# Kernel tuning notes

Hardware: AMD Instinct MI355X
Metric: run time of the kernel (lower is better)

The kernel has to match this reference:

```python
import jax, jax.numpy as jnp
import numpy as np

N = 4096      # num nodes
F = 64        # input feature dim
H = 8         # head_num
D = 8         # att_embedding_size


def setup_inputs() -> dict:
    key = jax.random.key(0)
    k1, k2, k3, k4, k5, k6 = jax.random.split(key, 6)
    X = jax.random.normal(k1, (N, F), dtype=jnp.float32)
    # sparse-ish binary adjacency with self loops (avg degree ~ 41)
    A = (jax.random.uniform(k2, (N, N)) < 0.01).astype(jnp.float32)
    A = jnp.maximum(A, jnp.eye(N, dtype=jnp.float32))
    # glorot-uniform-ish parameter init
    lim_w = np.sqrt(6.0 / (F + H * D)).astype(np.float32)
    W = jax.random.uniform(k3, (F, H * D), minval=-lim_w, maxval=lim_w, dtype=jnp.float32)
    lim_a = np.sqrt(6.0 / (1 + H * D)).astype(np.float32)
    att_self = jax.random.uniform(k4, (H, D), minval=-lim_a, maxval=lim_a, dtype=jnp.float32)
    att_neigh = jax.random.uniform(k5, (H, D), minval=-lim_a, maxval=lim_a, dtype=jnp.float32)
    bias = jnp.zeros((H, D), dtype=jnp.float32)
    return {"X": X, "A": A, "W": W, "att_self": att_self, "att_neigh": att_neigh, "bias": bias}


def reference(X, A, W, att_self, att_neigh, bias):
    # features: [N, H, D]
    feats = (X @ W).reshape(-1, H, D)
    # additive attention logits per node/head: [N, H]
    a_self = jnp.einsum('nhd,hd->nh', feats, att_self)
    a_neigh = jnp.einsum('nhd,hd->nh', feats, att_neigh)
    # scores[h, i, j] = a_self[i, h] + a_neigh[j, h]  -> [H, N, N]
    scores = a_self.T[:, :, None] + a_neigh.T[:, None, :]
    scores = jax.nn.leaky_relu(scores, negative_slope=0.2)
    # adjacency mask: -1e10 where no edge
    scores = scores + (-1e10 * (1.0 - A))[None, :, :]
    attn = jax.nn.softmax(scores, axis=-1)           # [H, N, N]
    # aggregate: [H, N, N] x [N, H, D] -> [N, H, D]
    out = jnp.einsum('hij,jhd->ihd', attn, feats)
    out = out + bias[None, :, :]                     # use_bias
    out = out.reshape(-1, H * D)                     # reduction='concat'
    return jax.nn.relu(out)                          # activation=relu
```

## Files before the change

### kernel.cpp

```cpp
#include <hip/hip_runtime.h>
#include <hip/hip_bf16.h>

#define NNODES 4096
#define NF 64
#define NH 8
#define ND 8
#define HD 64

__device__ __forceinline__ float ldv(const void* p, int i, bool f32) {
    return f32 ? ((const float*)p)[i]
               : __bfloat162float(((const __hip_bfloat16*)p)[i]);
}

__device__ __forceinline__ bool a_is_f32(const void* A) {
    return *(const unsigned int*)A == 0x3F800000u;
}

__global__ __launch_bounds__(256) void gat_feats(
    const void* __restrict__ X,
    const void* __restrict__ W,
    const void* __restrict__ att_self,
    const void* __restrict__ att_neigh,
    const void* __restrict__ A,
    float* __restrict__ feats,
    float* __restrict__ a_self,
    float* __restrict__ a_neigh)
{
    const bool f32 = a_is_f32(A);
    __shared__ float Wl[NF][HD];
    __shared__ float Xl[4][NF];

    const int t = threadIdx.x;

    #pragma unroll
    for (int k = 0; k < 16; ++k) {
        int idx = t + k * 256;
        Wl[idx >> 6][idx & 63] = ldv(W, idx, f32);
    }

    const int n0 = blockIdx.x * 4;
    const int r = t >> 6;
    const int c = t & 63;
    Xl[r][c] = ldv(X, (n0 + r) * NF + c, f32);
    __syncthreads();

    float acc = 0.f;
    #pragma unroll
    for (int k = 0; k < NF; ++k)
        acc = fmaf(Xl[r][k], Wl[k][c], acc);

    const int n = n0 + r;
    feats[n * HD + c] = acc;

    const int d = c & 7;
    const int h = c >> 3;
    float vs = acc * ldv(att_self, c, f32);
    float vn = acc * ldv(att_neigh, c, f32);
    #pragma unroll
    for (int off = 1; off < 8; off <<= 1) {
        vs += __shfl_xor(vs, off, 64);
        vn += __shfl_xor(vn, off, 64);
    }
    if (d == 0) {
        a_self[n * NH + h]  = vs;
        a_neigh[n * NH + h] = vn;
    }
}

__global__ __launch_bounds__(256) void gat_aggr(
    const void* __restrict__ A,
    const float* __restrict__ feats,
    const float* __restrict__ a_self_g,
    const float* __restrict__ a_neigh,
    const void* __restrict__ bias,
    float* __restrict__ out)
{
    const int i = blockIdx.x;
    const int t = threadIdx.x;
    const bool f32 = a_is_f32(A);
    const int wave = t >> 6, lane = t & 63;

    __shared__ unsigned short elist[NNODES];
    __shared__ int wtot[4];
    __shared__ float red[4][HD];
    __shared__ float dsh[4][NH];

    unsigned int bits = 0;
    if (f32) {
        const uint4* ap = (const uint4*)((const float*)A + (size_t)i * NNODES + t * 16);
        #pragma unroll
        for (int q = 0; q < 4; ++q) {
            uint4 p = ap[q];
            if (p.x) bits |= 1u << (4 * q + 0);
            if (p.y) bits |= 1u << (4 * q + 1);
            if (p.z) bits |= 1u << (4 * q + 2);
            if (p.w) bits |= 1u << (4 * q + 3);
        }
    } else {
        const uint4* ap = (const uint4*)((const unsigned short*)A + (size_t)i * NNODES + t * 16);
        uint4 p0 = ap[0], p1 = ap[1];
        unsigned int w0[4] = {p0.x, p0.y, p0.z, p0.w};
        unsigned int w1[4] = {p1.x, p1.y, p1.z, p1.w};
        #pragma unroll
        for (int q = 0; q < 4; ++q) {
            if (w0[q] & 0x0000ffffu) bits |= 1u << (2 * q);
            if (w0[q] & 0xffff0000u) bits |= 1u << (2 * q + 1);
            if (w1[q] & 0x0000ffffu) bits |= 1u << (8 + 2 * q);
            if (w1[q] & 0xffff0000u) bits |= 1u << (8 + 2 * q + 1);
        }
    }

    int cnt = __popc(bits);
    int incl = cnt;
    #pragma unroll
    for (int off = 1; off < 64; off <<= 1) {
        int nn = __shfl_up(incl, off, 64);
        if (lane >= off) incl += nn;
    }
    if (lane == 63) wtot[wave] = incl;
    __syncthreads();
    int base = 0;
    #pragma unroll
    for (int w = 0; w < 4; ++w) if (w < wave) base += wtot[w];
    const int nE = wtot[0] + wtot[1] + wtot[2] + wtot[3];
    int off0 = base + (incl - cnt);
    unsigned int mb = bits;
    while (mb) {
        int b = __ffs(mb) - 1; mb &= mb - 1;
        elist[off0++] = (unsigned short)(t * 16 + b);
    }
    __syncthreads();

    const int c = lane;
    const int h = c >> 3, d = c & 7;
    const float ash = a_self_g[i * NH + h];
    float acc = 0.f, den = 0.f;

    const int chunk = (nE + 3) >> 2;
    int e = wave * chunk;
    const int eEnd = min(nE, e + chunk);

    for (; e + 4 <= eEnd; e += 4) {
        int j0 = elist[e], j1 = elist[e + 1], j2 = elist[e + 2], j3 = elist[e + 3];
        float f0 = feats[j0 * HD + c];
        float f1 = feats[j1 * HD + c];
        float f2 = feats[j2 * HD + c];
        float f3 = feats[j3 * HD + c];
        float a0 = a_neigh[j0 * NH + h];
        float a1 = a_neigh[j1 * NH + h];
        float a2 = a_neigh[j2 * NH + h];
        float a3 = a_neigh[j3 * NH + h];
        float s0 = ash + a0; s0 = (s0 >= 0.f) ? s0 : 0.2f * s0; float w0 = __expf(s0);
        float s1 = ash + a1; s1 = (s1 >= 0.f) ? s1 : 0.2f * s1; float w1 = __expf(s1);
        float s2 = ash + a2; s2 = (s2 >= 0.f) ? s2 : 0.2f * s2; float w2 = __expf(s2);
        float s3 = ash + a3; s3 = (s3 >= 0.f) ? s3 : 0.2f * s3; float w3 = __expf(s3);
        acc = fmaf(w0, f0, acc);
        acc = fmaf(w1, f1, acc);
        acc = fmaf(w2, f2, acc);
        acc = fmaf(w3, f3, acc);
        den += (w0 + w1) + (w2 + w3);
    }
    for (; e < eEnd; ++e) {
        int j = elist[e];
        float s = ash + a_neigh[j * NH + h];
        s = (s >= 0.f) ? s : 0.2f * s;
        float wt = __expf(s);
        acc = fmaf(wt, feats[j * HD + c], acc);
        den += wt;
    }

    red[wave][c] = acc;
    if (d == 0) dsh[wave][h] = den;
    __syncthreads();

    if (t < HD) {
        float tot = red[0][t] + red[1][t] + red[2][t] + red[3][t];
        int hh = t >> 3;
        float dd = dsh[0][hh] + dsh[1][hh] + dsh[2][hh] + dsh[3][hh];
        float v = tot / dd + ldv(bias, t, f32);
        out[(size_t)i * HD + t] = fmaxf(v, 0.f);
    }
}

extern "C" void kernel_launch(void* const* d_in, const int* in_sizes, int n_in,
                              void* d_out, int out_size, void* d_ws, size_t ws_size,
                              hipStream_t stream) {
    const void* X         = d_in[0];
    const void* A         = d_in[1];
    const void* W         = d_in[2];
    const void* att_self  = d_in[3];
    const void* att_neigh = d_in[4];
    const void* bias      = d_in[5];
    float* out = (float*)d_out;

    float* feats   = (float*)d_ws;
    float* a_self  = feats  + NNODES * HD;
    float* a_neigh = a_self + NNODES * NH;

    gat_feats<<<NNODES / 4, 256, 0, stream>>>(X, W, att_self, att_neigh, A,
                                              feats, a_self, a_neigh);
    gat_aggr<<<NNODES, 256, 0, stream>>>(A, feats, a_self, a_neigh, bias, out);
}
```

Baseline: 29.93 us.

## Aggregate raw X per head then project through W, skip feats buffer

The first kernel now computes only the attention logits, by folding att vectors into W (U = W·att) so each node's logits are a 64-length dot with X. The aggregation kernel gathers neighbor X rows instead of precomputed feats, accumulates a per-head weighted sum of X (8 heads × 64 features), then multiplies by W held in shared memory. This removes the N×64 feats write/read, but each block now loads W and does an extra 8×64×64 matmul, with 8x more accumulator registers and more shared memory.

```diff
diff --git a/kernel.cpp b/kernel.cpp
--- a/kernel.cpp
+++ b/kernel.cpp
@@ -12,67 +12,78 @@
                : __bfloat162float(((const __hip_bfloat16*)p)[i]);
 }
 
+__device__ __forceinline__ void ld8(const void* base, int idx, bool f32, float* o) {
+    if (f32) {
+        const float4* p = (const float4*)((const float*)base + idx);
+        float4 a = p[0], b = p[1];
+        o[0]=a.x; o[1]=a.y; o[2]=a.z; o[3]=a.w;
+        o[4]=b.x; o[5]=b.y; o[6]=b.z; o[7]=b.w;
+    } else {
+        uint4 u = *(const uint4*)((const unsigned short*)base + idx);
+        unsigned int ws[4] = {u.x, u.y, u.z, u.w};
+        #pragma unroll
+        for (int q = 0; q < 4; ++q) {
+            o[2*q]   = __uint_as_float(ws[q] << 16);
+            o[2*q+1] = __uint_as_float(ws[q] & 0xffff0000u);
+        }
+    }
+}
+
 __device__ __forceinline__ bool a_is_f32(const void* A) {
     return *(const unsigned int*)A == 0x3F800000u;
 }
 
-__global__ __launch_bounds__(256) void gat_feats(
+__global__ __launch_bounds__(256) void gat_logits(
+    const void* __restrict__ X, const void* __restrict__ W,
+    const void* __restrict__ att_s, const void* __restrict__ att_n,
+    const void* __restrict__ A,
+    float* __restrict__ a_self, float* __restrict__ a_neigh)
+{
+    const bool f32 = a_is_f32(A);
+    __shared__ float UV[NF * 17];
+    __shared__ float Xl[16 * 65];
+    const int t = threadIdx.x;
+
+    #pragma unroll
+    for (int rep = 0; rep < 4; ++rep) {
+        int idx = t + rep * 256;
+        int f = idx >> 4, c6 = idx & 15;
+        int h = c6 & 7;
+        float wv[8];
+        ld8(W, f * HD + h * ND, f32, wv);
+        const void* att = (c6 < 8) ? att_s : att_n;
+        float s = 0.f;
+        #pragma unroll
+        for (int d = 0; d < 8; ++d)
+            s = fmaf(wv[d], ldv(att, h * 8 + d, f32), s);
+        UV[f * 17 + c6] = s;
+    }
+    if (t < 128) {
+        int row = t >> 3, col = (t & 7) * 8;
+        float xv[8];
+        ld8(X, (blockIdx.x * 16 + row) * NF + col, f32, xv);
+        #pragma unroll
+        for (int k = 0; k < 8; ++k) Xl[row * 65 + col + k] = xv[k];
+    }
+    __syncthreads();
+
+    const int r = t >> 4, c6 = t & 15;
+    float s = 0.f;
+    #pragma unroll
+    for (int f = 0; f < NF; ++f)
+        s = fmaf(Xl[r * 65 + f], UV[f * 17 + c6], s);
+    const int n = blockIdx.x * 16 + r;
+    if (c6 < 8) a_self[n * NH + c6]       = s;
+    else        a_neigh[n * NH + (c6-8)]  = s;
+}
+
+__global__ __launch_bounds__(256) void gat_aggr(
+    const void* __restrict__ A,
     const void* __restrict__ X,
     const void* __restrict__ W,
-    const void* __restrict__ att_self,
-    const void* __restrict__ att_neigh,
-    const void* __restrict__ A,
-    float* __restrict__ feats,
-    float* __restrict__ a_self,
-    float* __restrict__ a_neigh)
-{
-    const bool f32 = a_is_f32(A);
-    __shared__ float Wl[NF][HD];
-    __shared__ float Xl[4][NF];
-
-    const int t = threadIdx.x;
-
-    #pragma unroll
-    for (int k = 0; k < 16; ++k) {
-        int idx = t + k * 256;
-        Wl[idx >> 6][idx & 63] = ldv(W, idx, f32);
-    }
-
-    const int n0 = blockIdx.x * 4;
-    const int r = t >> 6;
-    const int c = t & 63;
-    Xl[r][c] = ldv(X, (n0 + r) * NF + c, f32);
-    __syncthreads();
-
-    float acc = 0.f;
-    #pragma unroll
-    for (int k = 0; k < NF; ++k)
-        acc = fmaf(Xl[r][k], Wl[k][c], acc);
-
-    const int n = n0 + r;
-    feats[n * HD + c] = acc;
-
-    const int d = c & 7;
-    const int h = c >> 3;
-    float vs = acc * ldv(att_self, c, f32);
-    float vn = acc * ldv(att_neigh, c, f32);
-    #pragma unroll
-    for (int off = 1; off < 8; off <<= 1) {
-        vs += __shfl_xor(vs, off, 64);
-        vn += __shfl_xor(vn, off, 64);
-    }
-    if (d == 0) {
-        a_self[n * NH + h]  = vs;
-        a_neigh[n * NH + h] = vn;
-    }
-}
-
-__global__ __launch_bounds__(256) void gat_aggr(
-    const void* __restrict__ A,
-    const float* __restrict__ feats,
+    const void* __restrict__ bias,
     const float* __restrict__ a_self_g,
     const float* __restrict__ a_neigh,
-    const void* __restrict__ bias,
     float* __restrict__ out)
 {
     const int i = blockIdx.x;
@@ -80,10 +91,23 @@
     const bool f32 = a_is_f32(A);
     const int wave = t >> 6, lane = t & 63;
 
-    __shared__ unsigned short elist[NNODES];
+    __shared__ float Wlf[NF * HD];
+    __shared__ float shbuf[2048];
+    __shared__ float agg[NH * 65];
+    __shared__ float dsh[4][NH];
+    __shared__ float denT[NH];
+    __shared__ float fin[4][HD];
     __shared__ int wtot[4];
-    __shared__ float red[4][HD];
-    __shared__ float dsh[4][NH];
+    unsigned short* elist = (unsigned short*)shbuf;
+    float* red = shbuf;
+
+    {
+        float wv[16];
+        ld8(W, t * 16,     f32, wv);
+        ld8(W, t * 16 + 8, f32, wv + 8);
+        #pragma unroll
+        for (int k = 0; k < 16; ++k) Wlf[t * 16 + k] = wv[k];
+    }
 
     unsigned int bits = 0;
     if (f32) {
@@ -91,10 +115,10 @@
         #pragma unroll
         for (int q = 0; q < 4; ++q) {
             uint4 p = ap[q];
-            if (p.x) bits |= 1u << (4 * q + 0);
-            if (p.y) bits |= 1u << (4 * q + 1);
-            if (p.z) bits |= 1u << (4 * q + 2);
-            if (p.w) bits |= 1u << (4 * q + 3);
+            if (p.x) bits |= 1u << (4*q+0);
+            if (p.y) bits |= 1u << (4*q+1);
+            if (p.z) bits |= 1u << (4*q+2);
+            if (p.w) bits |= 1u << (4*q+3);
         }
     } else {
         const uint4* ap = (const uint4*)((const unsigned short*)A + (size_t)i * NNODES + t * 16);
@@ -103,10 +127,10 @@
         unsigned int w1[4] = {p1.x, p1.y, p1.z, p1.w};
         #pragma unroll
         for (int q = 0; q < 4; ++q) {
-            if (w0[q] & 0x0000ffffu) bits |= 1u << (2 * q);
-            if (w0[q] & 0xffff0000u) bits |= 1u << (2 * q + 1);
-            if (w1[q] & 0x0000ffffu) bits |= 1u << (8 + 2 * q);
-            if (w1[q] & 0xffff0000u) bits |= 1u << (8 + 2 * q + 1);
+            if (w0[q] & 0x0000ffffu) bits |= 1u << (2*q);
+            if (w0[q] & 0xffff0000u) bits |= 1u << (2*q+1);
+            if (w1[q] & 0x0000ffffu) bits |= 1u << (8+2*q);
+            if (w1[q] & 0xffff0000u) bits |= 1u << (8+2*q+1);
         }
     }
 
@@ -131,53 +155,74 @@
     }
     __syncthreads();
 
-    const int c = lane;
-    const int h = c >> 3, d = c & 7;
+    const int h = lane >> 3, fs = lane & 7;
     const float ash = a_self_g[i * NH + h];
-    float acc = 0.f, den = 0.f;
+    float acc[8] = {0,0,0,0,0,0,0,0};
+    float den = 0.f;
 
     const int chunk = (nE + 3) >> 2;
     int e = wave * chunk;
     const int eEnd = min(nE, e + chunk);
 
-    for (; e + 4 <= eEnd; e += 4) {
-        int j0 = elist[e], j1 = elist[e + 1], j2 = elist[e + 2], j3 = elist[e + 3];
-        float f0 = feats[j0 * HD + c];
-        float f1 = feats[j1 * HD + c];
-        float f2 = feats[j2 * HD + c];
-        float f3 = feats[j3 * HD + c];
-        float a0 = a_neigh[j0 * NH + h];
-        float a1 = a_neigh[j1 * NH + h];
-        float a2 = a_neigh[j2 * NH + h];
-        float a3 = a_neigh[j3 * NH + h];
-        float s0 = ash + a0; s0 = (s0 >= 0.f) ? s0 : 0.2f * s0; float w0 = __expf(s0);
-        float s1 = ash + a1; s1 = (s1 >= 0.f) ? s1 : 0.2f * s1; float w1 = __expf(s1);
-        float s2 = ash + a2; s2 = (s2 >= 0.f) ? s2 : 0.2f * s2; float w2 = __expf(s2);
-        float s3 = ash + a3; s3 = (s3 >= 0.f) ? s3 : 0.2f * s3; float w3 = __expf(s3);
-        acc = fmaf(w0, f0, acc);
-        acc = fmaf(w1, f1, acc);
-        acc = fmaf(w2, f2, acc);
-        acc = fmaf(w3, f3, acc);
-        den += (w0 + w1) + (w2 + w3);
-    }
-    for (; e < eEnd; ++e) {
+    for (; e + 2 <= eEnd; e += 2) {
+        int j0 = elist[e], j1 = elist[e + 1];
+        float x0[8], x1[8];
+        ld8(X, j0 * NF + fs * 8, f32, x0);
+        ld8(X, j1 * NF + fs * 8, f32, x1);
+        float an0 = a_neigh[j0 * NH + h];
+        float an1 = a_neigh[j1 * NH + h];
+        float s0 = ash + an0; s0 = (s0 >= 0.f) ? s0 : 0.2f * s0; float w0 = __expf(s0);
+        float s1 = ash + an1; s1 = (s1 >= 0.f) ? s1 : 0.2f * s1; float w1 = __expf(s1);
+        #pragma unroll
+        for (int k = 0; k < 8; ++k) {
+            acc[k] = fmaf(w0, x0[k], acc[k]);
+            acc[k] = fmaf(w1, x1[k], acc[k]);
+        }
+        den += w0 + w1;
+    }
+    if (e < eEnd) {
         int j = elist[e];
+        float xv[8];
+        ld8(X, j * NF + fs * 8, f32, xv);
         float s = ash + a_neigh[j * NH + h];
         s = (s >= 0.f) ? s : 0.2f * s;
         float wt = __expf(s);
-        acc = fmaf(wt, feats[j * HD + c], acc);
+        #pragma unroll
+        for (int k = 0; k < 8; ++k) acc[k] = fmaf(wt, xv[k], acc[k]);
         den += wt;
     }
-
-    red[wave][c] = acc;
-    if (d == 0) dsh[wave][h] = den;
+    __syncthreads();
+
+    #pragma unroll
+    for (int k = 0; k < 8; ++k) red[wave * 512 + lane * 8 + k] = acc[k];
+    if (fs == 0) dsh[wave][h] = den;
+    __syncthreads();
+
+    #pragma unroll
+    for (int rr = 0; rr < 2; ++rr) {
+        int idx = t * 2 + rr;
+        int hh = idx >> 6, ff = idx & 63;
+        float v = red[idx] + red[512 + idx] + red[1024 + idx] + red[1536 + idx];
+        agg[hh * 65 + ff] = v;
+    }
+    if (t < NH) denT[t] = dsh[0][t] + dsh[1][t] + dsh[2][t] + dsh[3][t];
+    __syncthreads();
+
+    {
+        const int c = lane, hh = c >> 3;
+        float p = 0.f;
+        #pragma unroll
+        for (int f0 = 0; f0 < 16; ++f0) {
+            int f = wave * 16 + f0;
+            p = fmaf(agg[hh * 65 + f], Wlf[f * HD + c], p);
+        }
+        fin[wave][c] = p;
+    }
     __syncthreads();
 
     if (t < HD) {
-        float tot = red[0][t] + red[1][t] + red[2][t] + red[3][t];
-        int hh = t >> 3;
-        float dd = dsh[0][hh] + dsh[1][hh] + dsh[2][hh] + dsh[3][hh];
-        float v = tot / dd + ldv(bias, t, f32);
+        float tot = fin[0][t] + fin[1][t] + fin[2][t] + fin[3][t];
+        float v = tot / denT[t >> 3] + ldv(bias, t, f32);
         out[(size_t)i * HD + t] = fmaxf(v, 0.f);
     }
 }
@@ -193,11 +238,10 @@
     const void* bias      = d_in[5];
     float* out = (float*)d_out;
 
-    float* feats   = (float*)d_ws;
-    float* a_self  = feats  + NNODES * HD;
+    float* a_self  = (float*)d_ws;
     float* a_neigh = a_self + NNODES * NH;
 
-    gat_feats<<<NNODES / 4, 256, 0, stream>>>(X, W, att_self, att_neigh, A,
-                                              feats, a_self, a_neigh);
-    gat_aggr<<<NNODES, 256, 0, stream>>>(A, feats, a_self, a_neigh, bias, out);
-}
+    gat_logits<<<NNODES / 16, 256, 0, stream>>>(X, W, att_self, att_neigh, A,
+                                                a_self, a_neigh);
+    gat_aggr<<<NNODES, 256, 0, stream>>>(A, X, W, bias, a_self, a_neigh, out);
+}
```

Measured after the change: 38.82 us. +29.7%, slower.

## Process one node per wavefront using ballot-driven edge iteration without shared memory

Applied to the files above, without the earlier changes.

The aggregation kernel now assigns one destination row to each 64-lane wavefront instead of one row per 256-thread block. Each lane scans 64 adjacency entries into a 64-bit mask, and the edges are walked with ballot/shuffle bit iteration. This removes the shared-memory edge list, the prefix scan, the block barriers and the cross-wave reduction. The cost is that each wave processes all ~41 edges serially and each lane issues more adjacency loads, with less parallelism per row.

```diff
diff --git a/kernel.cpp b/kernel.cpp
--- a/kernel.cpp
+++ b/kernel.cpp
@@ -6,6 +6,8 @@
 #define NH 8
 #define ND 8
 #define HD 64
+
+typedef unsigned long long u64;
 
 __device__ __forceinline__ float ldv(const void* p, int i, bool f32) {
     return f32 ? ((const float*)p)[i]
@@ -75,111 +77,96 @@
     const void* __restrict__ bias,
     float* __restrict__ out)
 {
-    const int i = blockIdx.x;
-    const int t = threadIdx.x;
     const bool f32 = a_is_f32(A);
-    const int wave = t >> 6, lane = t & 63;
+    const int lane = threadIdx.x & 63;
+    const int i = (blockIdx.x << 2) + (threadIdx.x >> 6);
 
-    __shared__ unsigned short elist[NNODES];
-    __shared__ int wtot[4];
-    __shared__ float red[4][HD];
-    __shared__ float dsh[4][NH];
-
-    unsigned int bits = 0;
+    u64 bits = 0;
     if (f32) {
-        const uint4* ap = (const uint4*)((const float*)A + (size_t)i * NNODES + t * 16);
+        const uint4* ap = (const uint4*)((const float*)A + (size_t)i * NNODES + lane * 64);
         #pragma unroll
-        for (int q = 0; q < 4; ++q) {
-            uint4 p = ap[q];
-            if (p.x) bits |= 1u << (4 * q + 0);
-            if (p.y) bits |= 1u << (4 * q + 1);
-            if (p.z) bits |= 1u << (4 * q + 2);
-            if (p.w) bits |= 1u << (4 * q + 3);
+        for (int half = 0; half < 2; ++half) {
+            unsigned int mw = 0;
+            #pragma unroll
+            for (int q = 0; q < 8; ++q) {
+                uint4 p = ap[half * 8 + q];
+                if (p.x) mw |= 1u << (4 * q + 0);
+                if (p.y) mw |= 1u << (4 * q + 1);
+                if (p.z) mw |= 1u << (4 * q + 2);
+                if (p.w) mw |= 1u << (4 * q + 3);
+            }
+            bits |= (u64)mw << (32 * half);
         }
     } else {
-        const uint4* ap = (const uint4*)((const unsigned short*)A + (size_t)i * NNODES + t * 16);
-        uint4 p0 = ap[0], p1 = ap[1];
-        unsigned int w0[4] = {p0.x, p0.y, p0.z, p0.w};
-        unsigned int w1[4] = {p1.x, p1.y, p1.z, p1.w};
+        const uint4* ap = (const uint4*)((const unsigned short*)A + (size_t)i * NNODES + lane * 64);
         #pragma unroll
-        for (int q = 0; q < 4; ++q) {
-            if (w0[q] & 0x0000ffffu) bits |= 1u << (2 * q);
-            if (w0[q] & 0xffff0000u) bits |= 1u << (2 * q + 1);
-            if (w1[q] & 0x0000ffffu) bits |= 1u << (8 + 2 * q);
-            if (w1[q] & 0xffff0000u) bits |= 1u << (8 + 2 * q + 1);
+        for (int q = 0; q < 8; ++q) {
+            uint4 p = ap[q];
+            unsigned int w[4] = {p.x, p.y, p.z, p.w};
+            #pragma unroll
+            for (int r = 0; r < 4; ++r) {
+                int b = q * 8 + r * 2;
+                if (w[r] & 0x0000ffffu) bits |= 1ull << b;
+                if (w[r] & 0xffff0000u) bits |= 1ull << (b + 1);
+            }
         }
     }
 
-    int cnt = __popc(bits);
-    int incl = cnt;
-    #pragma unroll
-    for (int off = 1; off < 64; off <<= 1) {
-        int nn = __shfl_up(incl, off, 64);
-        if (lane >= off) incl += nn;
-    }
-    if (lane == 63) wtot[wave] = incl;
-    __syncthreads();
-    int base = 0;
-    #pragma unroll
-    for (int w = 0; w < 4; ++w) if (w < wave) base += wtot[w];
-    const int nE = wtot[0] + wtot[1] + wtot[2] + wtot[3];
-    int off0 = base + (incl - cnt);
-    unsigned int mb = bits;
-    while (mb) {
-        int b = __ffs(mb) - 1; mb &= mb - 1;
-        elist[off0++] = (unsigned short)(t * 16 + b);
-    }
-    __syncthreads();
+    u64 nz = __ballot(bits != 0);
+    u64 cur = 0;
+    int curbase = 0;
 
-    const int c = lane;
-    const int h = c >> 3, d = c & 7;
+    auto next_edge = [&]() -> int {
+        while (cur == 0) {
+            if (nz == 0) return -1;
+            int sl = __ffsll(nz) - 1;
+            nz &= nz - 1;
+            cur = __shfl(bits, sl, 64);
+            curbase = sl << 6;
+        }
+        int b = __ffsll(cur) - 1;
+        cur &= cur - 1;
+        return curbase + b;
+    };
+
+    const int c = lane, h = lane >> 3;
     const float ash = a_self_g[i * NH + h];
     float acc = 0.f, den = 0.f;
 
-    const int chunk = (nE + 3) >> 2;
-    int e = wave * chunk;
-    const int eEnd = min(nE, e + chunk);
+    for (;;) {
+        int j0 = next_edge();
+        if (j0 < 0) break;
+        int j1 = next_edge(); bool v1 = (j1 >= 0); j1 = v1 ? j1 : 0;
+        int j2 = next_edge(); bool v2 = (j2 >= 0); j2 = v2 ? j2 : 0;
+        int j3 = next_edge(); bool v3 = (j3 >= 0); j3 = v3 ? j3 : 0;
 
-    for (; e + 4 <= eEnd; e += 4) {
-        int j0 = elist[e], j1 = elist[e + 1], j2 = elist[e + 2], j3 = elist[e + 3];
+        float an0 = a_neigh[j0 * NH + h];
+        float an1 = a_neigh[j1 * NH + h];
+        float an2 = a_neigh[j2 * NH + h];
+        float an3 = a_neigh[j3 * NH + h];
         float f0 = feats[j0 * HD + c];
         float f1 = feats[j1 * HD + c];
         float f2 = feats[j2 * HD + c];
         float f3 = feats[j3 * HD + c];
-        float a0 = a_neigh[j0 * NH + h];
-        float a1 = a_neigh[j1 * NH + h];
-        float a2 = a_neigh[j2 * NH + h];
-        float a3 = a_neigh[j3 * NH + h];
-        float s0 = ash + a0; s0 = (s0 >= 0.f) ? s0 : 0.2f * s0; float w0 = __expf(s0);
-        float s1 = ash + a1; s1 = (s1 >= 0.f) ? s1 : 0.2f * s1; float w1 = __expf(s1);
-        float s2 = ash + a2; s2 = (s2 >= 0.f) ? s2 : 0.2f * s2; float w2 = __expf(s2);
-        float s3 = ash + a3; s3 = (s3 >= 0.f) ? s3 : 0.2f * s3; float w3 = __expf(s3);
+
+        if (!v1) an1 = -1e30f;
+        if (!v2) an2 = -1e30f;
+        if (!v3) an3 = -1e30f;
+
+        float s0 = ash + an0; s0 = (s0 >= 0.f) ? s0 : 0.2f * s0; float w0 = __expf(s0);
+        float s1 = ash + an1; s1 = (s1 >= 0.f) ? s1 : 0.2f * s1; float w1 = __expf(s1);
+        float s2 = ash + an2; s2 = (s2 >= 0.f) ? s2 : 0.2f * s2; float w2 = __expf(s2);
+        float s3 = ash + an3; s3 = (s3 >= 0.f) ? s3 : 0.2f * s3; float w3 = __expf(s3);
+
         acc = fmaf(w0, f0, acc);
         acc = fmaf(w1, f1, acc);
         acc = fmaf(w2, f2, acc);
         acc = fmaf(w3, f3, acc);
         den += (w0 + w1) + (w2 + w3);
     }
-    for (; e < eEnd; ++e) {
-        int j = elist[e];
-        float s = ash + a_neigh[j * NH + h];
-        s = (s >= 0.f) ? s : 0.2f * s;
-        float wt = __expf(s);
-        acc = fmaf(wt, feats[j * HD + c], acc);
-        den += wt;
-    }
 
-    red[wave][c] = acc;
-    if (d == 0) dsh[wave][h] = den;
-    __syncthreads();
-
-    if (t < HD) {
-        float tot = red[0][t] + red[1][t] + red[2][t] + red[3][t];
-        int hh = t >> 3;
-        float dd = dsh[0][hh] + dsh[1][hh] + dsh[2][hh] + dsh[3][hh];
-        float v = tot / dd + ldv(bias, t, f32);
-        out[(size_t)i * HD + t] = fmaxf(v, 0.f);
-    }
+    float v = acc / den + ldv(bias, c, f32);
+    out[(size_t)i * HD + c] = fmaxf(v, 0.f);
 }
 
 extern "C" void kernel_launch(void* const* d_in, const int* in_sizes, int n_in,
@@ -199,5 +186,5 @@
 
     gat_feats<<<NNODES / 4, 256, 0, stream>>>(X, W, att_self, att_neigh, A,
                                               feats, a_self, a_neigh);
-    gat_aggr<<<NNODES, 256, 0, stream>>>(A, feats, a_self, a_neigh, bias, out);
+    gat_aggr<<<NNODES / 4, 256, 0, stream>>>(A, feats, a_self, a_neigh, bias, out);
 }
```

Result: slower. 49.27 us (+64.6%).
